# Optimization experiments

Measured on AMD Instinct MI355X. Metric: run time of the kernel, lower is better.

## Reference

```python
import jax, jax.numpy as jnp
import numpy as np

B, D_MODEL, H, W = 4, 128, 128, 128
HEAD_DIM = 16
GROUP = D_MODEL // HEAD_DIM          # 8 deformable groups
D_INNER = D_MODEL                    # expand = 1
D_STATE = 1
DT_RANK = 8                          # ceil(d_model / 16)
D_CONV = 3
EPS = 1e-6


def setup_inputs() -> dict:
    key = jax.random.key(0)
    ks = jax.random.split(key, 10)
    f = jnp.float32
    # dt bias init as in DASSM.dt_init (dt in [1e-3, 1e-1], inverse-softplus)
    dt = jnp.exp(jax.random.uniform(ks[7], (D_INNER,), f)
                 * (np.log(0.1) - np.log(0.001)) + np.log(0.001))
    dt = jnp.clip(dt, 1e-4)
    dt_b = dt + jnp.log(-jnp.expm1(-dt))
    s = DT_RANK ** -0.5
    return dict(
        x=jax.random.normal(ks[0], (B, D_MODEL, H, W), f),
        in_proj_w=jax.random.normal(ks[1], (D_INNER, D_MODEL), f) * (D_MODEL ** -0.5),
        conv2d_w=jax.random.normal(ks[2], (D_INNER, 1, D_CONV, D_CONV), f) * 0.1,
        conv2d_b=jnp.zeros((D_INNER,), f),
        dw_w=jax.random.normal(ks[3], (D_INNER, 1, 3, 3), f) * 0.1,
        dw_b=jnp.zeros((D_INNER,), f),
        dw_ln_g=jnp.ones((D_INNER,), f),
        dw_ln_b=jnp.zeros((D_INNER,), f),
        off_w=jax.random.normal(ks[4], (GROUP * 2, D_INNER), f) * 0.01,
        off_b=jnp.zeros((GROUP * 2,), f),
        x_proj_w=jax.random.normal(ks[5], (DT_RANK + 2 * D_STATE, D_INNER), f) * (D_INNER ** -0.5),
        dt_w=jax.random.uniform(ks[6], (D_INNER, DT_RANK), f, -s, s),
        dt_b=dt_b,
        A_logs=jnp.tile(jnp.log(jnp.arange(1, D_STATE + 1, dtype=f))[None, :], (D_INNER, 1)),
        Ds=jnp.ones((D_INNER,), f),
        out_ln_g=jnp.ones((D_INNER,), f),
        out_ln_b=jnp.zeros((D_INNER,), f),
        out_proj_w=jax.random.normal(ks[8], (D_MODEL, D_INNER), f) * (D_INNER ** -0.5),
    )


def _layer_norm(x, g, b):
    m = x.mean(-1, keepdims=True)
    v = ((x - m) ** 2).mean(-1, keepdims=True)
    return (x - m) * jax.lax.rsqrt(v + EPS) * g + b


def _dwconv(x, w, b):
    # x: (B,C,H,W), w: (C,1,k,k) depthwise, 'SAME' == torch padding=(k-1)//2
    out = jax.lax.conv_general_dilated(
        x, w, (1, 1), 'SAME', feature_group_count=x.shape[1],
        dimension_numbers=('NCHW', 'OIHW', 'NCHW'))
    return out + b[None, :, None, None]


def _dcn_sample(img_last, offset):
    # DCNv3 with kernel_size=1, mask=1: sampling point = pixel center + offset.
    # img_last: (B,H,W,C); offset: (B,H,W,G*2) laid out (x,y) per group.
    b, h, w, c = img_last.shape
    gc = c // GROUP
    img = img_last.reshape(b, h, w, GROUP, gc)
    off = offset.reshape(b, h, w, GROUP, 2)
    px = jnp.arange(w, dtype=offset.dtype)[None, None, :, None] + off[..., 0]
    py = jnp.arange(h, dtype=offset.dtype)[None, :, None, None] + off[..., 1]
    y0 = jnp.floor(py)
    x0 = jnp.floor(px)
    wy = py - y0
    wx = px - x0
    bi = jnp.arange(b)[:, None, None, None]
    gi = jnp.arange(GROUP)[None, None, None, :]

    def tap(yi, xi, wgt):  # zero-padding bilinear tap (grid_sample, align_corners=False)
        valid = (yi >= 0) & (yi < h) & (xi >= 0) & (xi < w)
        yc = jnp.clip(yi, 0, h - 1).astype(jnp.int32)
        xc = jnp.clip(xi, 0, w - 1).astype(jnp.int32)
        v = img[bi, yc, xc, gi]  # (B,H,W,G,gc)
        return v * (wgt * valid)[..., None]

    out = (tap(y0, x0, (1 - wy) * (1 - wx)) + tap(y0, x0 + 1, (1 - wy) * wx)
           + tap(y0 + 1, x0, wy * (1 - wx)) + tap(y0 + 1, x0 + 1, wy * wx))
    return out.reshape(b, h, w, c)


def _selective_scan(xs, dts, A, Bs, Cs, Ds, dt_bias):
    # xs,dts: (B,D,L); A: (D,N); Bs,Cs: (B,N,L); delta_softplus=True
    delta = jax.nn.softplus(dts + dt_bias[None, :, None])
    dA = jnp.exp(jnp.einsum('bdl,dn->lbdn', delta, A))          # (L,B,D,N)
    dBx = jnp.einsum('bdl,bnl,bdl->lbdn', delta, Bs, xs)          # (L,B,D,N)
    C_t = jnp.transpose(Cs, (2, 0, 1))                            # (L,B,N)

    def step(hc, inputs):
        dA_t, dBx_t, c = inputs
        hc = dA_t * hc + dBx_t
        return hc, jnp.einsum('bdn,bn->bd', hc, c)

    h0 = jnp.zeros(dA.shape[1:], xs.dtype)
    _, ys = jax.lax.scan(step, h0, (dA, dBx, C_t))                # ys: (L,B,D)
    y = jnp.transpose(ys, (1, 2, 0))                              # (B,D,L)
    return y + Ds[None, :, None] * xs


def reference(x, in_proj_w, conv2d_w, conv2d_b, dw_w, dw_b, dw_ln_g, dw_ln_b,
              off_w, off_b, x_proj_w, dt_w, dt_b, A_logs, Ds,
              out_ln_g, out_ln_b, out_proj_w):
    # in_proj (1x1 conv, no bias) then depthwise conv + SiLU
    xin = jnp.einsum('bchw,oc->bohw', x, in_proj_w)
    xc = jax.nn.silu(_dwconv(xin, conv2d_w, conv2d_b))
    # Dynamic_Adaptive_Scan: dwconv -> LN(channels_last) -> GELU -> offsets -> DCNv3(k=1)
    x1 = _dwconv(xc, dw_w, dw_b)
    x1 = jax.nn.gelu(_layer_norm(jnp.transpose(x1, (0, 2, 3, 1)), dw_ln_g, dw_ln_b),
                     approximate=False)
    offset = x1 @ off_w.T + off_b                                  # (B,H,W,G*2)
    xd = _dcn_sample(jnp.transpose(xc, (0, 2, 3, 1)), offset)      # (B,H,W,C)
    xd = jnp.transpose(xd, (0, 3, 1, 2))                           # (B,C,H,W)
    # SSM (Mamba selective scan over L = H*W)
    Bn, C, Hh, Ww = xd.shape
    L = Hh * Ww
    xs = xd.reshape(Bn, C, L)
    x_dbl = jnp.einsum('rc,bcl->brl', x_proj_w, xs)
    dts, Bs, Cs = jnp.split(x_dbl, [DT_RANK, DT_RANK + D_STATE], axis=1)
    dts = jnp.einsum('dr,brl->bdl', dt_w, dts)
    A = -jnp.exp(A_logs)
    y = _selective_scan(xs, dts, A, Bs, Cs, Ds, dt_b).reshape(Bn, C, Hh, Ww)
    # out LayerNorm (over channels) + out_proj (1x1, no bias)
    y = jnp.transpose(_layer_norm(jnp.transpose(y, (0, 2, 3, 1)), out_ln_g, out_ln_b),
                      (0, 3, 1, 2))
    return jnp.einsum('bchw,oc->bohw', y, out_proj_w)
```

## Files before the change

### kernel.cpp

```cpp
#include <hip/hip_runtime.h>
#include <hip/hip_bf16.h>

typedef unsigned short u16;
typedef unsigned int u32;
typedef __bf16 bf16x8 __attribute__((ext_vector_type(8)));
typedef float f32x4 __attribute__((ext_vector_type(4)));

__device__ __forceinline__ float bfu(u16 u) { return __uint_as_float(((u32)u) << 16); }
__device__ __forceinline__ u16 fbf(float f) {
  __hip_bfloat16 h = __float2bfloat16(f);
  return *reinterpret_cast<u16*>(&h);
}
__device__ __forceinline__ float softplusf(float z) {
  float t = __expf(z);
  return (z > 20.f) ? z : __logf(1.f + t);
}
__device__ __forceinline__ float lo16(u32 p) { return __uint_as_float(p << 16); }
__device__ __forceinline__ float hi16(u32 p) { return __uint_as_float(p & 0xffff0000u); }
__device__ __forceinline__ bf16x8 ld_bf8(const u16* p) {
  union { uint4 u; bf16x8 v; } c;
  c.u = *(const uint4*)p;
  return c.v;
}

__global__ __launch_bounds__(256) void k_inproj(const float* __restrict__ X,
                                                const float* __restrict__ W,
                                                u16* __restrict__ out) {
  __shared__ __align__(16) u16 Ws[128 * 136];
  __shared__ __align__(16) u16 Xs[64 * 136];
  int tid = threadIdx.x;
  int b = blockIdx.x >> 8;
  int l0 = (blockIdx.x & 255) << 6;
  for (int i = 0; i < 16; ++i) {
    int idx = (i << 8) + tid;
    int o = idx >> 5, c4 = (idx & 31) << 2;
    float4 w4 = *(const float4*)&W[(o << 7) + c4];
    ushort4 s;
    s.x = fbf(w4.x); s.y = fbf(w4.y); s.z = fbf(w4.z); s.w = fbf(w4.w);
    *(ushort4*)&Ws[o * 136 + c4] = s;
  }
  for (int i = 0; i < 8; ++i) {
    int idx = (i << 8) + tid;
    int c = idx >> 4, lq = (idx & 15) << 2;
    float4 x4 = *(const float4*)&X[(((long)(b << 7) + c) << 14) + l0 + lq];
    Xs[(lq + 0) * 136 + c] = fbf(x4.x);
    Xs[(lq + 1) * 136 + c] = fbf(x4.y);
    Xs[(lq + 2) * 136 + c] = fbf(x4.z);
    Xs[(lq + 3) * 136 + c] = fbf(x4.w);
  }
  __syncthreads();
  int w = tid >> 6, lane = tid & 63;
  int mrow = lane & 15, quad = lane >> 4;
  f32x4 acc[2][4];
#pragma unroll
  for (int ot = 0; ot < 2; ++ot)
#pragma unroll
    for (int lt = 0; lt < 4; ++lt) acc[ot][lt] = (f32x4){0.f, 0.f, 0.f, 0.f};
#pragma unroll
  for (int kb = 0; kb < 4; ++kb) {
    int c0 = (kb << 5) + (quad << 3);
    bf16x8 af[2], bfr[4];
#pragma unroll
    for (int ot = 0; ot < 2; ++ot)
      af[ot] = ld_bf8(&Ws[((w << 5) + (ot << 4) + mrow) * 136 + c0]);
#pragma unroll
    for (int lt = 0; lt < 4; ++lt)
      bfr[lt] = ld_bf8(&Xs[((lt << 4) + mrow) * 136 + c0]);
#pragma unroll
    for (int ot = 0; ot < 2; ++ot)
#pragma unroll
      for (int lt = 0; lt < 4; ++lt)
        acc[ot][lt] = __builtin_amdgcn_mfma_f32_16x16x32_bf16(af[ot], bfr[lt], acc[ot][lt], 0, 0, 0);
  }
#pragma unroll
  for (int ot = 0; ot < 2; ++ot)
#pragma unroll
    for (int lt = 0; lt < 4; ++lt) {
      int l = l0 + (lt << 4) + mrow;
      int o = (w << 5) + (ot << 4) + (quad << 2);
      ushort4 s;
      s.x = fbf(acc[ot][lt][0]); s.y = fbf(acc[ot][lt][1]);
      s.z = fbf(acc[ot][lt][2]); s.w = fbf(acc[ot][lt][3]);
      *(ushort4*)&out[(((long)(b << 14) + l) << 7) + o] = s;
    }
}

__global__ __launch_bounds__(256) void k_dwconv(const u16* __restrict__ in,
                                                const float* __restrict__ w9,
                                                const float* __restrict__ bias,
                                                u16* __restrict__ out, int act) {
  __shared__ float wsT[9][128];
  __shared__ float bs[128];
  int tid = threadIdx.x;
  for (int i = 0; i < 5; ++i) {
    int lin = (i << 8) + tid;
    if (lin < 1152) { int c = lin / 9, k = lin - 9 * c; wsT[k][c] = w9[lin]; }
  }
  if (tid < 128) bs[tid] = bias[tid];
  __syncthreads();
  int blk = blockIdx.x;
  int b = blk >> 10;
  int s = blk & 1023;
  int h = s >> 3;
  int w = ((s & 7) << 4) + (tid >> 4);
  int c0 = (tid & 15) << 3;
  const u16* bbase = in + ((long)b << 21);
  float acc[8];
  {
    float4 b0 = *(const float4*)&bs[c0];
    float4 b1 = *(const float4*)&bs[c0 + 4];
    acc[0] = b0.x; acc[1] = b0.y; acc[2] = b0.z; acc[3] = b0.w;
    acc[4] = b1.x; acc[5] = b1.y; acc[6] = b1.z; acc[7] = b1.w;
  }
#pragma unroll
  for (int ky = -1; ky <= 1; ++ky) {
    int y = h + ky;
    if ((unsigned)y >= 128u) continue;
#pragma unroll
    for (int kx = -1; kx <= 1; ++kx) {
      int x = w + kx;
      if ((unsigned)x >= 128u) continue;
      int k = (ky + 1) * 3 + (kx + 1);
      uint4 v = *(const uint4*)(bbase + ((((y << 7) + x)) << 7) + c0);
      float4 w0 = *(const float4*)&wsT[k][c0];
      float4 w1 = *(const float4*)&wsT[k][c0 + 4];
      u32 vv[4] = {v.x, v.y, v.z, v.w};
      float wf[8] = {w0.x, w0.y, w0.z, w0.w, w1.x, w1.y, w1.z, w1.w};
#pragma unroll
      for (int cc = 0; cc < 8; ++cc) {
        float xv = (cc & 1) ? hi16(vv[cc >> 1]) : lo16(vv[cc >> 1]);
        acc[cc] = fmaf(wf[cc], xv, acc[cc]);
      }
    }
  }
  if (act) {
#pragma unroll
    for (int cc = 0; cc < 8; ++cc) acc[cc] = acc[cc] / (1.f + __expf(-acc[cc]));
  }
  ushort4 s0, s1;
  s0.x = fbf(acc[0]); s0.y = fbf(acc[1]); s0.z = fbf(acc[2]); s0.w = fbf(acc[3]);
  s1.x = fbf(acc[4]); s1.y = fbf(acc[5]); s1.z = fbf(acc[6]); s1.w = fbf(acc[7]);
  u16* po = out + ((long)b << 21) + ((((h << 7) + w)) << 7) + c0;
  *(ushort4*)po = s0;
  *(ushort4*)(po + 4) = s1;
}

__global__ __launch_bounds__(256) void k_offset(const u16* __restrict__ x1,
                                                const float* __restrict__ g,
                                                const float* __restrict__ bt,
                                                const float* __restrict__ offw,
                                                const float* __restrict__ offb,
                                                float* __restrict__ offs) {
  __shared__ __align__(16) u16 Ge[64 * 136];
  __shared__ __align__(16) u16 Wos[16 * 136];
  __shared__ float ps[4][64], pss[4][64];
  __shared__ float mean_s[64], rstd_s[64];
  __shared__ float gs[128], bsh[128];
  int tid = threadIdx.x;
  int pg0 = blockIdx.x << 6;
  int b = pg0 >> 14;
  if (tid < 128) { gs[tid] = g[tid]; bsh[tid] = bt[tid]; }
  for (int i = 0; i < 8; ++i) {
    int idx = (i << 8) + tid;
    int o = idx >> 7, c = idx & 127;
    Wos[o * 136 + c] = fbf(offw[idx]);
  }
  int l = tid >> 2, cq = (tid & 3) << 5;
  {
    const u16* px = x1 + (((long)(pg0 + l)) << 7) + cq;
    float s = 0.f, ss = 0.f;
#pragma unroll
    for (int i2 = 0; i2 < 4; ++i2) {
      uint4 v = *(const uint4*)(px + (i2 << 3));
      *(uint4*)&Ge[l * 136 + cq + (i2 << 3)] = v;
      u32 vv[4] = {v.x, v.y, v.z, v.w};
#pragma unroll
      for (int cc = 0; cc < 8; ++cc) {
        float xv = (cc & 1) ? hi16(vv[cc >> 1]) : lo16(vv[cc >> 1]);
        s += xv; ss = fmaf(xv, xv, ss);
      }
    }
    ps[tid & 3][l] = s; pss[tid & 3][l] = ss;
  }
  __syncthreads();
  if (tid < 64) {
    float s = ps[0][tid] + ps[1][tid] + ps[2][tid] + ps[3][tid];
    float ss = pss[0][tid] + pss[1][tid] + pss[2][tid] + pss[3][tid];
    float m = s * (1.f / 128.f);
    mean_s[tid] = m;
    rstd_s[tid] = rsqrtf(ss * (1.f / 128.f) - m * m + 1e-6f);
  }
  __syncthreads();
  {
    float m = mean_s[l], r = rstd_s[l];
    u16* row = &Ge[l * 136 + cq];
#pragma unroll 8
    for (int cc = 0; cc < 32; ++cc) {
      int c = cq + cc;
      float v = bfu(row[cc]);
      float xn = fmaf((v - m) * r, gs[c], bsh[c]);
      row[cc] = fbf(0.5f * xn * (1.f + erff(xn * 0.70710678118f)));
    }
  }
  __syncthreads();
  int w = tid >> 6, lane = tid & 63;
  int mrow = lane & 15, quad = lane >> 4;
  f32x4 acc0 = (f32x4){0.f, 0.f, 0.f, 0.f};
#pragma unroll
  for (int kb = 0; kb < 4; ++kb) {
    int c0 = (kb << 5) + (quad << 3);
    bf16x8 af = ld_bf8(&Wos[mrow * 136 + c0]);
    bf16x8 bfr = ld_bf8(&Ge[((w << 4) + mrow) * 136 + c0]);
    acc0 = __builtin_amdgcn_mfma_f32_16x16x32_bf16(af, bfr, acc0, 0, 0, 0);
  }
  int lg = (pg0 & 16383) + (w << 4) + mrow;
  float2* po = (float2*)offs;
  int o0 = quad << 2;
  po[(((long)((b << 3) + (quad << 1))) << 14) + lg] =
      make_float2(acc0[0] + offb[o0], acc0[1] + offb[o0 + 1]);
  po[(((long)((b << 3) + (quad << 1) + 1)) << 14) + lg] =
      make_float2(acc0[2] + offb[o0 + 2], acc0[3] + offb[o0 + 3]);
}

__global__ __launch_bounds__(512) void k_dcn(const u16* __restrict__ xc,
                                             const float* __restrict__ offs,
                                             const float* __restrict__ xpw,
                                             const float* __restrict__ dtw,
                                             u16* __restrict__ xs,
                                             u16* __restrict__ dts,
                                             float* __restrict__ Bsb,
                                             float* __restrict__ Csb) {
  __shared__ float xds[64 * 129];
  __shared__ float xdbl[64 * 13];
  __shared__ float xpws[1280];
  __shared__ float dtws[1024];
  int tid = threadIdx.x;
  for (int i = 0; i < 3; ++i) { int idx = (i << 9) + tid; if (idx < 1280) xpws[idx] = xpw[idx]; }
  for (int i = 0; i < 2; ++i) { int idx = (i << 9) + tid; dtws[idx] = dtw[idx]; }
  int blk = blockIdx.x;
  int b = blk >> 8;
  int l0 = (blk & 255) << 6;
  int p = tid & 63, gg = tid >> 6;
  int l = l0 + p, hh = l >> 7, ww = l & 127;
  float2 off = ((const float2*)offs)[(((long)((b << 3) + gg)) << 14) + l];
  float px = (float)ww + off.x, py = (float)hh + off.y;
  float x0f = floorf(px), y0f = floorf(py);
  float wx = px - x0f, wy = py - y0f;
  int ix = (int)x0f, iy = (int)y0f;
  float acc[16];
#pragma unroll
  for (int ch = 0; ch < 16; ++ch) acc[ch] = 0.f;
  const u16* bbase = xc + ((long)b << 21) + (gg << 4);
  int xi[4] = {ix, ix + 1, ix, ix + 1};
  int yi[4] = {iy, iy, iy + 1, iy + 1};
  float wt4[4] = {(1.f - wy) * (1.f - wx), (1.f - wy) * wx, wy * (1.f - wx), wy * wx};
#pragma unroll
  for (int t = 0; t < 4; ++t) {
    if (wt4[t] != 0.f && (unsigned)yi[t] < 128u && (unsigned)xi[t] < 128u) {
      const u16* pp = bbase + ((((yi[t] << 7) + xi[t])) << 7);
      uint4 v0 = *(const uint4*)pp;
      uint4 v1 = *(const uint4*)(pp + 8);
      float wv = wt4[t];
      u32 vv[8] = {v0.x, v0.y, v0.z, v0.w, v1.x, v1.y, v1.z, v1.w};
#pragma unroll
      for (int ch = 0; ch < 16; ++ch) {
        float xv = (ch & 1) ? hi16(vv[ch >> 1]) : lo16(vv[ch >> 1]);
        acc[ch] = fmaf(wv, xv, acc[ch]);
      }
    }
  }
#pragma unroll
  for (int ch = 0; ch < 16; ++ch) xds[p * 129 + (gg << 4) + ch] = acc[ch];
  __syncthreads();
#pragma unroll
  for (int it = 0; it < 2; ++it) {
    int task = (it << 9) + tid;
    int cc = task >> 3, t = task & 7;
    u32 pk[4];
#pragma unroll
    for (int jj = 0; jj < 4; ++jj) {
      u16 a0 = fbf(xds[((t << 3) + 2 * jj + 0) * 129 + cc]);
      u16 a1 = fbf(xds[((t << 3) + 2 * jj + 1) * 129 + cc]);
      pk[jj] = (u32)a0 | ((u32)a1 << 16);
    }
    *(uint4*)&xs[(((long)(b << 7) + cc) << 14) + l0 + (t << 3)] =
        make_uint4(pk[0], pk[1], pk[2], pk[3]);
  }
  for (int task = tid; task < 640; task += 512) {
    int p2 = task / 10, r = task - p2 * 10;
    const float* wr = xpws + (r << 7);
    const float* xr = xds + p2 * 129;
    float sacc = 0.f;
#pragma unroll 8
    for (int cc = 0; cc < 128; ++cc) sacc = fmaf(wr[cc], xr[cc], sacc);
    xdbl[p2 * 13 + r] = sacc;
  }
  __syncthreads();
#pragma unroll
  for (int it = 0; it < 2; ++it) {
    int task = (it << 9) + tid;
    int dd = task >> 3, t = task & 7;
    const float* wd = dtws + (dd << 3);
    u32 pk[4];
#pragma unroll
    for (int jj = 0; jj < 4; ++jj) {
      u16 h2[2];
#pragma unroll
      for (int hh2 = 0; hh2 < 2; ++hh2) {
        const float* xb = xdbl + ((t << 3) + 2 * jj + hh2) * 13;
        float sacc = 0.f;
#pragma unroll
        for (int r = 0; r < 8; ++r) sacc = fmaf(wd[r], xb[r], sacc);
        h2[hh2] = fbf(sacc);
      }
      pk[jj] = (u32)h2[0] | ((u32)h2[1] << 16);
    }
    *(uint4*)&dts[(((long)(b << 7) + dd) << 14) + l0 + (t << 3)] =
        make_uint4(pk[0], pk[1], pk[2], pk[3]);
  }
  if (tid < 64) {
    Bsb[((long)b << 14) + l0 + tid] = xdbl[tid * 13 + 8];
    Csb[((long)b << 14) + l0 + tid] = xdbl[tid * 13 + 9];
  }
}

__global__ __launch_bounds__(1024) void k_scan(u16* __restrict__ xy,
                                               const u16* __restrict__ dts16,
                                               const float* __restrict__ Bsb,
                                               const float* __restrict__ Csb,
                                               const float* __restrict__ A_logs,
                                               const float* __restrict__ Dsv,
                                               const float* __restrict__ dtbv) {
  __shared__ float swp[16], swe[16];
  int bd = blockIdx.x;
  int b = bd >> 7, d = bd & 127;
  float Ad = -__expf(A_logs[d]);
  float dtb = dtbv[d];
  float Dd = Dsv[d];
  int t = threadIdx.x;
  int lane = t & 63, wid = t >> 6;
  long base = ((long)bd << 14) + (t << 4);
  long bb = ((long)b << 14) + (t << 4);
  const uint4* pz4 = (const uint4*)(dts16 + base);
  const uint4* px4 = (const uint4*)(xy + base);
  const float4* pB = (const float4*)(Bsb + bb);
  const float4* pC = (const float4*)(Csb + bb);
  uint4 zA = pz4[0], zB = pz4[1];
  uint4 xA = px4[0], xB = px4[1];
  u32 zw[8] = {zA.x, zA.y, zA.z, zA.w, zB.x, zB.y, zB.z, zB.w};
  u32 xw[8] = {xA.x, xA.y, xA.z, xA.w, xB.x, xB.y, xB.z, xB.w};
  float E = 0.f, P = 1.f;
#pragma unroll
  for (int q = 0; q < 4; ++q) {
    float4 B4 = pB[q];
    float Bq[4] = {B4.x, B4.y, B4.z, B4.w};
#pragma unroll
    for (int j = 0; j < 4; ++j) {
      int k = (q << 2) + j;
      float z = (k & 1) ? hi16(zw[k >> 1]) : lo16(zw[k >> 1]);
      float xv = (k & 1) ? hi16(xw[k >> 1]) : lo16(xw[k >> 1]);
      float delta = softplusf(z + dtb);
      float a = __expf(delta * Ad);
      E = fmaf(a, E, delta * Bq[j] * xv);
      P *= a;
    }
  }
#pragma unroll
  for (int off = 1; off < 64; off <<= 1) {
    float Pp = __shfl_up(P, off);
    float Ep = __shfl_up(E, off);
    if (lane >= off) { E = fmaf(P, Ep, E); P *= Pp; }
  }
  if (lane == 63) { swp[wid] = P; swe[wid] = E; }
  __syncthreads();
  if (t < 16) {
    float p2 = swp[t], e2 = swe[t];
#pragma unroll
    for (int off = 1; off < 16; off <<= 1) {
      float pp = __shfl_up(p2, off);
      float ee = __shfl_up(e2, off);
      if (t >= off) { e2 = fmaf(p2, ee, e2); p2 *= pp; }
    }
    swp[t] = p2; swe[t] = e2;
  }
  __syncthreads();
  float hw = (wid == 0) ? 0.f : swe[wid - 1];
  float Pex = __shfl_up(P, 1);
  float Eex = __shfl_up(E, 1);
  if (lane == 0) { Pex = 1.f; Eex = 0.f; }
  float h = fmaf(Pex, hw, Eex);
  u32 ypk[8];
#pragma unroll
  for (int q = 0; q < 4; ++q) {
    float4 B4 = pB[q];
    float4 C4 = pC[q];
    float Bq[4] = {B4.x, B4.y, B4.z, B4.w};
    float Cq[4] = {C4.x, C4.y, C4.z, C4.w};
#pragma unroll
    for (int j = 0; j < 4; ++j) {
      int k = (q << 2) + j;
      float z = (k & 1) ? hi16(zw[k >> 1]) : lo16(zw[k >> 1]);
      float xv = (k & 1) ? hi16(xw[k >> 1]) : lo16(xw[k >> 1]);
      float delta = softplusf(z + dtb);
      float a = __expf(delta * Ad);
      h = fmaf(a, h, delta * Bq[j] * xv);
      u16 yb = fbf(fmaf(Dd, xv, h * Cq[j]));
      if ((k & 1) == 0) ypk[k >> 1] = yb; else ypk[k >> 1] |= (u32)yb << 16;
    }
  }
  uint4* py = (uint4*)(xy + base);
  py[0] = make_uint4(ypk[0], ypk[1], ypk[2], ypk[3]);
  py[1] = make_uint4(ypk[4], ypk[5], ypk[6], ypk[7]);
}

__global__ void k_sums(const float* __restrict__ W2, const float* __restrict__ g,
                       const float* __restrict__ bln, float* __restrict__ s12) {
  int o = threadIdx.x;
  float s1 = 0.f, s2 = 0.f;
  for (int c = 0; c < 128; ++c) {
    float w = W2[(o << 7) + c];
    s1 = fmaf(w, bln[c], s1);
    s2 = fmaf(w, g[c], s2);
  }
  s12[o] = s1;
  s12[128 + o] = s2;
}

__global__ __launch_bounds__(256) void k_outproj(const u16* __restrict__ y,
                                                 const float* __restrict__ W2,
                                                 const float* __restrict__ g,
                                                 const float* __restrict__ s12,
                                                 float* __restrict__ out) {
  __shared__ __align__(16) u16 Ws[128 * 136];
  __shared__ __align__(16) u16 Ys[64 * 136];
  __shared__ float ps[4][64], pss[4][64];
  __shared__ float mean_s[64], rstd_s[64];
  int tid = threadIdx.x;
  int b = blockIdx.x >> 8;
  int l0 = (blockIdx.x & 255) << 6;
  for (int i = 0; i < 16; ++i) {
    int idx = (i << 8) + tid;
    int o = idx >> 5, c4 = (idx & 31) << 2;
    float4 w4 = *(const float4*)&W2[(o << 7) + c4];
    ushort4 s;
    s.x = fbf(w4.x * g[c4]);     s.y = fbf(w4.y * g[c4 + 1]);
    s.z = fbf(w4.z * g[c4 + 2]); s.w = fbf(w4.w * g[c4 + 3]);
    *(ushort4*)&Ws[o * 136 + c4] = s;
  }
  for (int i = 0; i < 4; ++i) {
    int idx = (i << 8) + tid;
    int c = idx >> 3, lq = (idx & 7) << 3;
    uint4 v = *(const uint4*)&y[(((long)(b << 7) + c) << 14) + l0 + lq];
    u32 vv[4] = {v.x, v.y, v.z, v.w};
#pragma unroll
    for (int r = 0; r < 8; ++r)
      Ys[(lq + r) * 136 + c] = (u16)((r & 1) ? (vv[r >> 1] >> 16) : (vv[r >> 1] & 0xffffu));
  }
  __syncthreads();
  {
    int l = tid & 63, q = tid >> 6;
    const u16* row = &Ys[l * 136 + (q << 5)];
    float s = 0.f, ss = 0.f;
#pragma unroll 8
    for (int c = 0; c < 32; ++c) { float v = bfu(row[c]); s += v; ss = fmaf(v, v, ss); }
    ps[q][l] = s; pss[q][l] = ss;
  }
  __syncthreads();
  if (tid < 64) {
    float s = ps[0][tid] + ps[1][tid] + ps[2][tid] + ps[3][tid];
    float ss = pss[0][tid] + pss[1][tid] + pss[2][tid] + pss[3][tid];
    float m = s * (1.f / 128.f);
    mean_s[tid] = m;
    rstd_s[tid] = rsqrtf(ss * (1.f / 128.f) - m * m + 1e-6f);
  }
  __syncthreads();
  int w = tid >> 6, lane = tid & 63;
  int mrow = lane & 15, quad = lane >> 4;
  f32x4 acc[2][4];
#pragma unroll
  for (int ot = 0; ot < 2; ++ot)
#pragma unroll
    for (int lt = 0; lt < 4; ++lt) acc[ot][lt] = (f32x4){0.f, 0.f, 0.f, 0.f};
#pragma unroll
  for (int kb = 0; kb < 4; ++kb) {
    int c0 = (kb << 5) + (quad << 3);
    bf16x8 af[2], bfr[4];
#pragma unroll
    for (int ot = 0; ot < 2; ++ot)
      af[ot] = ld_bf8(&Ws[((w << 5) + (ot << 4) + mrow) * 136 + c0]);
#pragma unroll
    for (int lt = 0; lt < 4; ++lt)
      bfr[lt] = ld_bf8(&Ys[((lt << 4) + mrow) * 136 + c0]);
#pragma unroll
    for (int ot = 0; ot < 2; ++ot)
#pragma unroll
      for (int lt = 0; lt < 4; ++lt)
        acc[ot][lt] = __builtin_amdgcn_mfma_f32_16x16x32_bf16(af[ot], bfr[lt], acc[ot][lt], 0, 0, 0);
  }
  float s1r[2][4], s2r[2][4];
#pragma unroll
  for (int ot = 0; ot < 2; ++ot)
#pragma unroll
    for (int r = 0; r < 4; ++r) {
      int o = (w << 5) + (ot << 4) + (quad << 2) + r;
      s1r[ot][r] = s12[o];
      s2r[ot][r] = s12[128 + o];
    }
#pragma unroll
  for (int ot = 0; ot < 2; ++ot)
#pragma unroll
    for (int lt = 0; lt < 4; ++lt) {
      int lcol = (lt << 4) + mrow;
      float mv = mean_s[lcol], rv = rstd_s[lcol];
      int obase = (w << 5) + (ot << 4) + (quad << 2);
#pragma unroll
      for (int r = 0; r < 4; ++r) {
        float v = fmaf(rv, acc[ot][lt][r] - mv * s2r[ot][r], s1r[ot][r]);
        out[(((long)(b << 7) + obase + r) << 14) + l0 + lcol] = v;
      }
    }
}

extern "C" void kernel_launch(void* const* d_in, const int* in_sizes, int n_in,
                              void* d_out, int out_size, void* d_ws, size_t ws_size,
                              hipStream_t stream) {
  const float* x         = (const float*)d_in[0];
  const float* in_proj_w = (const float*)d_in[1];
  const float* conv2d_w  = (const float*)d_in[2];
  const float* conv2d_b  = (const float*)d_in[3];
  const float* dw_w      = (const float*)d_in[4];
  const float* dw_b      = (const float*)d_in[5];
  const float* dw_ln_g   = (const float*)d_in[6];
  const float* dw_ln_b   = (const float*)d_in[7];
  const float* off_w     = (const float*)d_in[8];
  const float* off_b     = (const float*)d_in[9];
  const float* x_proj_w  = (const float*)d_in[10];
  const float* dt_w      = (const float*)d_in[11];
  const float* dt_b      = (const float*)d_in[12];
  const float* A_logs    = (const float*)d_in[13];
  const float* Ds        = (const float*)d_in[14];
  const float* out_ln_g  = (const float*)d_in[15];
  const float* out_ln_b  = (const float*)d_in[16];
  const float* out_proj_w= (const float*)d_in[17];
  float* out = (float*)d_out;

  u16* A  = (u16*)d_ws;
  u16* Bx = A + 8388608;
  u16* Dd = Bx + 8388608;
  float* offs  = (float*)(Dd + 8388608);
  float* Bsb   = offs + 1048576;
  float* Csb   = Bsb + 65536;
  float* s12   = Csb + 65536;

  hipLaunchKernelGGL(k_inproj, dim3(1024), dim3(256), 0, stream, x, in_proj_w, A);
  hipLaunchKernelGGL(k_dwconv, dim3(4096), dim3(256), 0, stream, A, conv2d_w, conv2d_b, Bx, 1);
  hipLaunchKernelGGL(k_dwconv, dim3(4096), dim3(256), 0, stream, Bx, dw_w, dw_b, A, 0);
  hipLaunchKernelGGL(k_offset, dim3(1024), dim3(256), 0, stream, A, dw_ln_g, dw_ln_b, off_w, off_b, offs);
  hipLaunchKernelGGL(k_dcn, dim3(1024), dim3(512), 0, stream, Bx, offs, x_proj_w, dt_w, A, Dd, Bsb, Csb);
  hipLaunchKernelGGL(k_scan, dim3(512), dim3(1024), 0, stream, A, Dd, Bsb, Csb, A_logs, Ds, dt_b);
  hipLaunchKernelGGL(k_sums, dim3(1), dim3(128), 0, stream, out_proj_w, out_ln_g, out_ln_b, s12);
  hipLaunchKernelGGL(k_outproj, dim3(1024), dim3(256), 0, stream, A, out_proj_w, out_ln_g, s12, out);
}
```

Before: 234.8 us.

## Restructure DCN kernel: register-level x_proj partials, bf16 staging, transposed dt projection

The k_dcn kernel now computes the x_proj projection straight from per-thread sampled registers as 16-channel partial sums, then reduces 8 partials per output. It no longer re-reads a 128-wide fp32 shared row per dot product. Sampled values are staged in shared memory as bf16 instead of fp32, and the dt projection uses transposed weights and activations so each thread computes two rows of 8 outputs with vector loads. The goals are less shared-memory traffic, a smaller LDS footprint for higher occupancy (launch bounds 512,6), and fewer redundant FMAs. The cost is extra partial-sum storage and global weight reads from each thread.

```diff
diff --git a/kernel.cpp b/kernel.cpp
--- a/kernel.cpp
+++ b/kernel.cpp
@@ -222,21 +222,24 @@
       make_float2(acc0[2] + offb[o0 + 2], acc0[3] + offb[o0 + 3]);
 }
 
-__global__ __launch_bounds__(512) void k_dcn(const u16* __restrict__ xc,
-                                             const float* __restrict__ offs,
-                                             const float* __restrict__ xpw,
-                                             const float* __restrict__ dtw,
-                                             u16* __restrict__ xs,
-                                             u16* __restrict__ dts,
-                                             float* __restrict__ Bsb,
-                                             float* __restrict__ Csb) {
-  __shared__ float xds[64 * 129];
-  __shared__ float xdbl[64 * 13];
-  __shared__ float xpws[1280];
-  __shared__ float dtws[1024];
+__global__ __launch_bounds__(512, 6) void k_dcn(const u16* __restrict__ xc,
+                                                const float* __restrict__ offs,
+                                                const float* __restrict__ xpw,
+                                                const float* __restrict__ dtw,
+                                                u16* __restrict__ xs,
+                                                u16* __restrict__ dts,
+                                                float* __restrict__ Bsb,
+                                                float* __restrict__ Csb) {
+  __shared__ __align__(16) u16 xds_bf[64 * 132];
+  __shared__ float part[64 * 81];
+  __shared__ __align__(16) float xdblT[8 * 64];
+  __shared__ float dtwsT[8 * 128];
   int tid = threadIdx.x;
-  for (int i = 0; i < 3; ++i) { int idx = (i << 9) + tid; if (idx < 1280) xpws[idx] = xpw[idx]; }
-  for (int i = 0; i < 2; ++i) { int idx = (i << 9) + tid; dtws[idx] = dtw[idx]; }
+  for (int i = 0; i < 2; ++i) {
+    int idx = (i << 9) + tid;
+    int dd2 = idx >> 3, r = idx & 7;
+    dtwsT[(r << 7) + dd2] = dtw[idx];
+  }
   int blk = blockIdx.x;
   int b = blk >> 8;
   int l0 = (blk & 255) << 6;
@@ -269,9 +272,44 @@
       }
     }
   }
-#pragma unroll
-  for (int ch = 0; ch < 16; ++ch) xds[p * 129 + (gg << 4) + ch] = acc[ch];
-  __syncthreads();
+  {
+    u32 pk[8];
+#pragma unroll
+    for (int j = 0; j < 8; ++j)
+      pk[j] = (u32)fbf(acc[2 * j]) | ((u32)fbf(acc[2 * j + 1]) << 16);
+    u16* row = &xds_bf[p * 132 + (gg << 4)];
+#pragma unroll
+    for (int q = 0; q < 4; ++q)
+      *(uint2*)(row + (q << 2)) = make_uint2(pk[2 * q], pk[2 * q + 1]);
+  }
+  {
+    int ggu = __builtin_amdgcn_readfirstlane(gg);
+    const float* wb = xpw + (ggu << 4);
+    int pbase = p * 81 + gg;
+#pragma unroll
+    for (int r = 0; r < 10; ++r) {
+      const float* wr = wb + (r << 7);
+      float s = 0.f;
+#pragma unroll
+      for (int ch = 0; ch < 16; ++ch) s = fmaf(wr[ch], acc[ch], s);
+      part[pbase + (r << 3)] = s;
+    }
+  }
+  __syncthreads();
+  {
+    int task = tid;
+#pragma unroll
+    for (int pass = 0; pass < 2; ++pass, task += 512) {
+      if (task < 640) {
+        int r = task >> 6, p2 = task & 63;
+        const float* pp = &part[p2 * 81 + (r << 3)];
+        float s = ((pp[0] + pp[1]) + (pp[2] + pp[3])) + ((pp[4] + pp[5]) + (pp[6] + pp[7]));
+        if (r < 8) xdblT[(r << 6) + p2] = s;
+        else if (r == 8) Bsb[((long)b << 14) + l0 + p2] = s;
+        else Csb[((long)b << 14) + l0 + p2] = s;
+      }
+    }
+  }
 #pragma unroll
   for (int it = 0; it < 2; ++it) {
     int task = (it << 9) + tid;
@@ -279,48 +317,43 @@
     u32 pk[4];
 #pragma unroll
     for (int jj = 0; jj < 4; ++jj) {
-      u16 a0 = fbf(xds[((t << 3) + 2 * jj + 0) * 129 + cc]);
-      u16 a1 = fbf(xds[((t << 3) + 2 * jj + 1) * 129 + cc]);
+      u16 a0 = xds_bf[((t << 3) + 2 * jj + 0) * 132 + cc];
+      u16 a1 = xds_bf[((t << 3) + 2 * jj + 1) * 132 + cc];
       pk[jj] = (u32)a0 | ((u32)a1 << 16);
     }
     *(uint4*)&xs[(((long)(b << 7) + cc) << 14) + l0 + (t << 3)] =
         make_uint4(pk[0], pk[1], pk[2], pk[3]);
   }
-  for (int task = tid; task < 640; task += 512) {
-    int p2 = task / 10, r = task - p2 * 10;
-    const float* wr = xpws + (r << 7);
-    const float* xr = xds + p2 * 129;
-    float sacc = 0.f;
-#pragma unroll 8
-    for (int cc = 0; cc < 128; ++cc) sacc = fmaf(wr[cc], xr[cc], sacc);
-    xdbl[p2 * 13 + r] = sacc;
-  }
-  __syncthreads();
-#pragma unroll
-  for (int it = 0; it < 2; ++it) {
-    int task = (it << 9) + tid;
-    int dd = task >> 3, t = task & 7;
-    const float* wd = dtws + (dd << 3);
-    u32 pk[4];
+  __syncthreads();
+  {
+    int dd = tid >> 3, t = tid & 7;
+    float y0[8], y1[8];
+#pragma unroll
+    for (int j = 0; j < 8; ++j) { y0[j] = 0.f; y1[j] = 0.f; }
+#pragma unroll
+    for (int r = 0; r < 8; ++r) {
+      float w0 = dtwsT[(r << 7) + dd];
+      float w1 = dtwsT[(r << 7) + dd + 64];
+      const float* xr = &xdblT[(r << 6) + (t << 3)];
+      float4 xa = *(const float4*)xr;
+      float4 xb = *(const float4*)(xr + 4);
+      float xv[8] = {xa.x, xa.y, xa.z, xa.w, xb.x, xb.y, xb.z, xb.w};
+#pragma unroll
+      for (int j = 0; j < 8; ++j) {
+        y0[j] = fmaf(w0, xv[j], y0[j]);
+        y1[j] = fmaf(w1, xv[j], y1[j]);
+      }
+    }
+    u32 pk0[4], pk1[4];
 #pragma unroll
     for (int jj = 0; jj < 4; ++jj) {
-      u16 h2[2];
-#pragma unroll
-      for (int hh2 = 0; hh2 < 2; ++hh2) {
-        const float* xb = xdbl + ((t << 3) + 2 * jj + hh2) * 13;
-        float sacc = 0.f;
-#pragma unroll
-        for (int r = 0; r < 8; ++r) sacc = fmaf(wd[r], xb[r], sacc);
-        h2[hh2] = fbf(sacc);
-      }
-      pk[jj] = (u32)h2[0] | ((u32)h2[1] << 16);
+      pk0[jj] = (u32)fbf(y0[2 * jj]) | ((u32)fbf(y0[2 * jj + 1]) << 16);
+      pk1[jj] = (u32)fbf(y1[2 * jj]) | ((u32)fbf(y1[2 * jj + 1]) << 16);
     }
     *(uint4*)&dts[(((long)(b << 7) + dd) << 14) + l0 + (t << 3)] =
-        make_uint4(pk[0], pk[1], pk[2], pk[3]);
-  }
-  if (tid < 64) {
-    Bsb[((long)b << 14) + l0 + tid] = xdbl[tid * 13 + 8];
-    Csb[((long)b << 14) + l0 + tid] = xdbl[tid * 13 + 9];
+        make_uint4(pk0[0], pk0[1], pk0[2], pk0[3]);
+    *(uint4*)&dts[(((long)(b << 7) + dd + 64) << 14) + l0 + (t << 3)] =
+        make_uint4(pk1[0], pk1[1], pk1[2], pk1[3]);
   }
 }
 
```

New measurement: 224.6 us. -4.4%, faster.
